# Kernel tuning notes

Measured on AMD Instinct MI355X. Metric: run time of the kernel, lower is better.

Reference implementation:

```python
import jax, jax.numpy as jnp
import numpy as np

NUM_CAPSULE = 10
DIM_CAPSULE = 16
NUM_ROUTING = 3
EPS = 1e-7  # tf.keras.backend.epsilon()


def squash(v, axis=-1):
    s2 = jnp.sum(jnp.square(v), axis=axis, keepdims=True)
    scale = s2 / (1.0 + s2) / jnp.sqrt(s2 + EPS)
    return scale * v


def setup_inputs() -> dict:
    key = jax.random.key(0)
    k1, k2 = jax.random.split(key)
    B, in_dim = 16384, 2048
    inputs = jax.random.normal(k1, (B, in_dim), dtype=jnp.float32)
    # glorot-uniform-ish scale for the kernel
    limit = np.sqrt(6.0 / (in_dim + NUM_CAPSULE * DIM_CAPSULE)).astype(np.float32)
    kernel = jax.random.uniform(k2, (in_dim, NUM_CAPSULE * DIM_CAPSULE),
                                dtype=jnp.float32, minval=-limit, maxval=limit)
    return {"inputs": inputs, "kernel": kernel}


def reference(inputs, kernel):
    B = inputs.shape[0]
    # [B, in_dim] @ [in_dim, nc*dc] -> [B, nc, dc]
    inputs_hat = (inputs @ kernel).reshape(B, NUM_CAPSULE, DIM_CAPSULE)
    b = jnp.zeros((B, NUM_CAPSULE, 1), dtype=inputs.dtype)
    outputs = None
    for _ in range(NUM_ROUTING):
        c = jax.nn.softmax(b, axis=1)                      # [B, nc, 1]
        s = jnp.sum(c * inputs_hat, axis=1, keepdims=True)  # [B, 1, dc]
        outputs = squash(s)                                 # [B, 1, dc]
        # matmul(inputs_hat, outputs, transpose_b=True) -> [B, nc, 1]
        b = b + jnp.einsum('bnd,bd->bn', inputs_hat, outputs[:, 0, :])[:, :, None]
    return outputs[:, 0, :]  # [B, dc]
```

## Files before the change

### kernel.cpp

```cpp
#include <hip/hip_runtime.h>
#include <hip/hip_bf16.h>

typedef unsigned int u32;
typedef unsigned short u16;
typedef __attribute__((ext_vector_type(8))) __bf16 bf16x8;
typedef __attribute__((ext_vector_type(4))) float f32x4;

#define N_CAP 10
#define D_CAP 16
#define NN 160
#define KK 2048
#define BM 64
#define BK 32
#define NSTEPS (KK / BK)
#define THREADS 640
#define LDST 40
#define AS_TILE (BM * LDST)
#define HAT_STRIDE 164
#define SMEM_BYTES (BM * HAT_STRIDE * 4)

__device__ __forceinline__ u32 pack_hi(float f0, float f1) {
  u32 u0 = __builtin_bit_cast(u32, f0), u1 = __builtin_bit_cast(u32, f1);
  return (u0 >> 16) | (u1 & 0xFFFF0000u);
}
__device__ __forceinline__ float hi_part(float f) {
  u32 u = __builtin_bit_cast(u32, f) & 0xFFFF0000u;
  return __builtin_bit_cast(float, u);
}
union U4B8 { uint4 u; bf16x8 b; };

__global__ __launch_bounds__(THREADS, 3) void capsule_fused(
    const float* __restrict__ X, const float* __restrict__ W, float* __restrict__ out) {
  __shared__ __align__(16) char smem[SMEM_BYTES];
  u16* As_hi = (u16*)smem;
  u16* As_lo = As_hi + AS_TILE;
  float* hat = (float*)smem;

  const int t = threadIdx.x;
  const int rbase = blockIdx.x * BM;
  const int lane = t & 63;
  const int w = t >> 6;
  const int wip = (w >= 5) ? 1 : 0;
  const int wjp = w - 5 * wip;
  const int l15 = lane & 15;
  const int q = lane >> 4;

  const int ar = t >> 2;
  const int ak = (t & 3) * 8;
  const float* gA = X + (size_t)(rbase + ar) * KK + ak;

  const float* gB = W + (q * 8) * NN + 32 * wjp + l15;

  f32x4 acc00 = {0.f,0.f,0.f,0.f}, acc01 = {0.f,0.f,0.f,0.f};
  f32x4 acc10 = {0.f,0.f,0.f,0.f}, acc11 = {0.f,0.f,0.f,0.f};

  float4 pa0A, pa1A, pa0B, pa1B;
  if (t < 256) {
    pa0A = *(const float4*)(gA);            pa1A = *(const float4*)(gA + 4);
    pa0B = *(const float4*)(gA + BK);       pa1B = *(const float4*)(gA + BK + 4);
  }
  float buA[16], buB[16];
#pragma unroll
  for (int j = 0; j < 8; ++j) { buA[j] = gB[j * NN]; buA[8 + j] = gB[16 + j * NN]; }

#define STEP(S, PA0, PA1, BU, BNXT)                                              \
  {                                                                              \
    __syncthreads();                            \
    if (t < 256) {                                                               \
      uint4 hi, lo;                                                              \
      hi.x = pack_hi(PA0.x, PA0.y); hi.y = pack_hi(PA0.z, PA0.w);                \
      hi.z = pack_hi(PA1.x, PA1.y); hi.w = pack_hi(PA1.z, PA1.w);                \
      float l0 = PA0.x - hi_part(PA0.x), l1 = PA0.y - hi_part(PA0.y);            \
      float l2 = PA0.z - hi_part(PA0.z), l3 = PA0.w - hi_part(PA0.w);            \
      float l4 = PA1.x - hi_part(PA1.x), l5 = PA1.y - hi_part(PA1.y);            \
      float l6 = PA1.z - hi_part(PA1.z), l7 = PA1.w - hi_part(PA1.w);            \
      lo.x = pack_hi(l0, l1); lo.y = pack_hi(l2, l3);                            \
      lo.z = pack_hi(l4, l5); lo.w = pack_hi(l6, l7);                            \
      *(uint4*)(As_hi + ar * LDST + ak) = hi;                                    \
      *(uint4*)(As_lo + ar * LDST + ak) = lo;                                    \
    }                                                                            \
    __syncthreads();                                             \
    if (t < 256 && (S) + 2 < NSTEPS) {                                           \
      PA0 = *(const float4*)(gA + ((S) + 2) * BK);                               \
      PA1 = *(const float4*)(gA + ((S) + 2) * BK + 4);                           \
    }                                                                            \
    if ((S) + 1 < NSTEPS) {                                                      \
      const float* b = gB + ((S) + 1) * (BK * NN);                               \
      _Pragma("unroll")                                                          \
      for (int j = 0; j < 8; ++j) { BNXT[j] = b[j * NN]; BNXT[8 + j] = b[16 + j * NN]; } \
    }                                                                            \
    U4B8 bh0, bl0, bh1, bl1;                                                     \
    bh0.u.x = pack_hi(BU[0], BU[1]);  bh0.u.y = pack_hi(BU[2], BU[3]);           \
    bh0.u.z = pack_hi(BU[4], BU[5]);  bh0.u.w = pack_hi(BU[6], BU[7]);           \
    bh1.u.x = pack_hi(BU[8], BU[9]);  bh1.u.y = pack_hi(BU[10], BU[11]);         \
    bh1.u.z = pack_hi(BU[12], BU[13]); bh1.u.w = pack_hi(BU[14], BU[15]);        \
    float lb[16];                                                                \
    _Pragma("unroll")                                                            \
    for (int j = 0; j < 16; ++j) lb[j] = BU[j] - hi_part(BU[j]);                 \
    bl0.u.x = pack_hi(lb[0], lb[1]);  bl0.u.y = pack_hi(lb[2], lb[3]);           \
    bl0.u.z = pack_hi(lb[4], lb[5]);  bl0.u.w = pack_hi(lb[6], lb[7]);           \
    bl1.u.x = pack_hi(lb[8], lb[9]);  bl1.u.y = pack_hi(lb[10], lb[11]);         \
    bl1.u.z = pack_hi(lb[12], lb[13]); bl1.u.w = pack_hi(lb[14], lb[15]);        \
    bf16x8 ah0 = *(const bf16x8*)(As_hi + (32 * wip + l15) * LDST + q * 8);      \
    bf16x8 ah1 = *(const bf16x8*)(As_hi + (32 * wip + 16 + l15) * LDST + q * 8); \
    bf16x8 al0 = *(const bf16x8*)(As_lo + (32 * wip + l15) * LDST + q * 8);      \
    bf16x8 al1 = *(const bf16x8*)(As_lo + (32 * wip + 16 + l15) * LDST + q * 8); \
    acc00 = __builtin_amdgcn_mfma_f32_16x16x32_bf16(ah0, bh0.b, acc00, 0, 0, 0); \
    acc00 = __builtin_amdgcn_mfma_f32_16x16x32_bf16(ah0, bl0.b, acc00, 0, 0, 0); \
    acc00 = __builtin_amdgcn_mfma_f32_16x16x32_bf16(al0, bh0.b, acc00, 0, 0, 0); \
    acc01 = __builtin_amdgcn_mfma_f32_16x16x32_bf16(ah0, bh1.b, acc01, 0, 0, 0); \
    acc01 = __builtin_amdgcn_mfma_f32_16x16x32_bf16(ah0, bl1.b, acc01, 0, 0, 0); \
    acc01 = __builtin_amdgcn_mfma_f32_16x16x32_bf16(al0, bh1.b, acc01, 0, 0, 0); \
    acc10 = __builtin_amdgcn_mfma_f32_16x16x32_bf16(ah1, bh0.b, acc10, 0, 0, 0); \
    acc10 = __builtin_amdgcn_mfma_f32_16x16x32_bf16(ah1, bl0.b, acc10, 0, 0, 0); \
    acc10 = __builtin_amdgcn_mfma_f32_16x16x32_bf16(al1, bh0.b, acc10, 0, 0, 0); \
    acc11 = __builtin_amdgcn_mfma_f32_16x16x32_bf16(ah1, bh1.b, acc11, 0, 0, 0); \
    acc11 = __builtin_amdgcn_mfma_f32_16x16x32_bf16(ah1, bl1.b, acc11, 0, 0, 0); \
    acc11 = __builtin_amdgcn_mfma_f32_16x16x32_bf16(al1, bh1.b, acc11, 0, 0, 0); \
  }

  for (int s = 0; s < NSTEPS; s += 2) {
    STEP(s,     pa0A, pa1A, buA, buB)
    STEP(s + 1, pa0B, pa1B, buB, buA)
  }
#undef STEP

  __syncthreads();
#pragma unroll
  for (int r = 0; r < 4; ++r) {
    const int rowb = 32 * wip + 4 * q + r;
    const int colb = 32 * wjp + l15;
    hat[rowb * HAT_STRIDE + colb]             = acc00[r];
    hat[rowb * HAT_STRIDE + colb + 16]        = acc01[r];
    hat[(rowb + 16) * HAT_STRIDE + colb]      = acc10[r];
    hat[(rowb + 16) * HAT_STRIDE + colb + 16] = acc11[r];
  }
  __syncthreads();

  if (t < BM) {
    const int r = t;
    float bb[N_CAP];
#pragma unroll
    for (int n = 0; n < N_CAP; ++n) bb[n] = 0.f;
    float v[D_CAP];
#pragma unroll
    for (int it = 0; it < 3; ++it) {
      float mx = bb[0];
#pragma unroll
      for (int n = 1; n < N_CAP; ++n) mx = fmaxf(mx, bb[n]);
      float c[N_CAP], se = 0.f;
#pragma unroll
      for (int n = 0; n < N_CAP; ++n) { c[n] = __expf(bb[n] - mx); se += c[n]; }
      const float inv = 1.f / se;
      float sd[D_CAP], s2 = 0.f;
#pragma unroll
      for (int d = 0; d < D_CAP; ++d) {
        float x = 0.f;
#pragma unroll
        for (int n = 0; n < N_CAP; ++n) x += c[n] * hat[r * HAT_STRIDE + n * D_CAP + d];
        x *= inv;
        sd[d] = x;
        s2 += x * x;
      }
      const float scale = s2 / ((1.f + s2) * sqrtf(s2 + 1e-7f));
#pragma unroll
      for (int d = 0; d < D_CAP; ++d) v[d] = scale * sd[d];
      if (it < 2) {
#pragma unroll
        for (int n = 0; n < N_CAP; ++n) {
          float dd = 0.f;
#pragma unroll
          for (int d = 0; d < D_CAP; ++d) dd += hat[r * HAT_STRIDE + n * D_CAP + d] * v[d];
          bb[n] += dd;
        }
      }
    }
#pragma unroll
    for (int d = 0; d < D_CAP; ++d)
      out[(size_t)(rbase + r) * D_CAP + d] = v[d];
  }
}

extern "C" void kernel_launch(void* const* d_in, const int* in_sizes, int n_in,
                              void* d_out, int out_size, void* d_ws, size_t ws_size,
                              hipStream_t stream) {
  const float* X = (const float*)d_in[0];
  const float* W = (const float*)d_in[1];
  if (n_in >= 2 && in_sizes[0] == KK * NN) {
    X = (const float*)d_in[1];
    W = (const float*)d_in[0];
  }
  capsule_fused<<<16384 / BM, THREADS, 0, stream>>>(X, W, (float*)d_out);
}
```

Baseline: 242.9 us.

## Prepack W into bf16 hi/lo fragments and load A directly without LDS

Adds a pre-kernel that splits W into bf16 hi/lo pairs laid out in MFMA fragment order in a global buffer, so the main kernel loads B fragments with vector loads instead of strided scalar loads and per-step packing. The A operand is now read per wave straight from global into registers, which removes the LDS staging and both barriers per k-step, at the cost of redundant A reads across the five column waves. The routing epilogue is spread over 8 threads per row using shuffle reductions, and occupancy hint drops to 2. The pack kernel runs on every call and adds a second launch.

```diff
diff --git a/kernel.cpp b/kernel.cpp
--- a/kernel.cpp
+++ b/kernel.cpp
@@ -1,5 +1,4 @@
 #include <hip/hip_runtime.h>
-#include <hip/hip_bf16.h>
 
 typedef unsigned int u32;
 typedef unsigned short u16;
@@ -11,13 +10,12 @@
 #define NN 160
 #define KK 2048
 #define BM 64
-#define BK 32
-#define NSTEPS (KK / BK)
+#define NSTEPS 64
 #define THREADS 640
-#define LDST 40
-#define AS_TILE (BM * LDST)
-#define HAT_STRIDE 164
-#define SMEM_BYTES (BM * HAT_STRIDE * 4)
+#define HAT_STRIDE 165
+#define BSTEP 20480
+
+__device__ __align__(16) unsigned char Wpack_g[NSTEPS * BSTEP];
 
 __device__ __forceinline__ u32 pack_hi(float f0, float f1) {
   u32 u0 = __builtin_bit_cast(u32, f0), u1 = __builtin_bit_cast(u32, f1);
@@ -29,12 +27,31 @@
 }
 union U4B8 { uint4 u; bf16x8 b; };
 
-__global__ __launch_bounds__(THREADS, 3) void capsule_fused(
-    const float* __restrict__ X, const float* __restrict__ W, float* __restrict__ out) {
-  __shared__ __align__(16) char smem[SMEM_BYTES];
-  u16* As_hi = (u16*)smem;
-  u16* As_lo = As_hi + AS_TILE;
-  float* hat = (float*)smem;
+__global__ void pack_w(const float* __restrict__ W) {
+  const int tid = blockIdx.x * 256 + threadIdx.x;
+  if (tid >= NSTEPS * 5 * 64 * 4) return;
+  const int v = tid & 3;
+  const int lane = (tid >> 2) & 63;
+  const int sw = tid >> 8;
+  const int wjp = sw % 5;
+  const int s = sw / 5;
+  const int col = 32 * wjp + 16 * (v & 1) + (lane & 15);
+  const int kb = 32 * s + 8 * (lane >> 4);
+  u32 r[4];
+#pragma unroll
+  for (int jj = 0; jj < 4; ++jj) {
+    float x0 = W[(size_t)(kb + 2 * jj) * NN + col];
+    float x1 = W[(size_t)(kb + 2 * jj + 1) * NN + col];
+    if (v >= 2) { x0 -= hi_part(x0); x1 -= hi_part(x1); }
+    r[jj] = pack_hi(x0, x1);
+  }
+  uint4 o; o.x = r[0]; o.y = r[1]; o.z = r[2]; o.w = r[3];
+  *(uint4*)(Wpack_g + (size_t)tid * 16) = o;
+}
+
+__global__ __launch_bounds__(THREADS, 2) void capsule_fused(
+    const float* __restrict__ X, float* __restrict__ out) {
+  __shared__ float hat[BM * HAT_STRIDE];
 
   const int t = threadIdx.x;
   const int rbase = blockIdx.x * BM;
@@ -45,87 +62,76 @@
   const int l15 = lane & 15;
   const int q = lane >> 4;
 
-  const int ar = t >> 2;
-  const int ak = (t & 3) * 8;
-  const float* gA = X + (size_t)(rbase + ar) * KK + ak;
-
-  const float* gB = W + (q * 8) * NN + 32 * wjp + l15;
+  const float* pA0 = X + (size_t)(rbase + 32 * wip + l15) * KK + 8 * q;
+  const float* pA1 = pA0 + 16 * KK;
+  const unsigned char* pB = Wpack_g + ((size_t)wjp * 64 + lane) * 64;
 
   f32x4 acc00 = {0.f,0.f,0.f,0.f}, acc01 = {0.f,0.f,0.f,0.f};
   f32x4 acc10 = {0.f,0.f,0.f,0.f}, acc11 = {0.f,0.f,0.f,0.f};
 
-  float4 pa0A, pa1A, pa0B, pa1B;
-  if (t < 256) {
-    pa0A = *(const float4*)(gA);            pa1A = *(const float4*)(gA + 4);
-    pa0B = *(const float4*)(gA + BK);       pa1B = *(const float4*)(gA + BK + 4);
-  }
-  float buA[16], buB[16];
-#pragma unroll
-  for (int j = 0; j < 8; ++j) { buA[j] = gB[j * NN]; buA[8 + j] = gB[16 + j * NN]; }
-
-#define STEP(S, PA0, PA1, BU, BNXT)                                              \
+  float4 aE0, aE1, aE2, aE3, aO0, aO1, aO2, aO3;
+  uint4 bE0, bE1, bE2, bE3, bO0, bO1, bO2, bO3;
+
+  aE0 = *(const float4*)(pA0);      aE1 = *(const float4*)(pA0 + 4);
+  aE2 = *(const float4*)(pA1);      aE3 = *(const float4*)(pA1 + 4);
+  aO0 = *(const float4*)(pA0 + 32); aO1 = *(const float4*)(pA0 + 36);
+  aO2 = *(const float4*)(pA1 + 32); aO3 = *(const float4*)(pA1 + 36);
+  bE0 = *(const uint4*)(pB);        bE1 = *(const uint4*)(pB + 16);
+  bE2 = *(const uint4*)(pB + 32);   bE3 = *(const uint4*)(pB + 48);
+
+#define STEP(S, A0, A1, A2, A3, BC0, BC1, BC2, BC3, BN0, BN1, BN2, BN3)          \
   {                                                                              \
-    __syncthreads();                            \
-    if (t < 256) {                                                               \
-      uint4 hi, lo;                                                              \
-      hi.x = pack_hi(PA0.x, PA0.y); hi.y = pack_hi(PA0.z, PA0.w);                \
-      hi.z = pack_hi(PA1.x, PA1.y); hi.w = pack_hi(PA1.z, PA1.w);                \
-      float l0 = PA0.x - hi_part(PA0.x), l1 = PA0.y - hi_part(PA0.y);            \
-      float l2 = PA0.z - hi_part(PA0.z), l3 = PA0.w - hi_part(PA0.w);            \
-      float l4 = PA1.x - hi_part(PA1.x), l5 = PA1.y - hi_part(PA1.y);            \
-      float l6 = PA1.z - hi_part(PA1.z), l7 = PA1.w - hi_part(PA1.w);            \
-      lo.x = pack_hi(l0, l1); lo.y = pack_hi(l2, l3);                            \
-      lo.z = pack_hi(l4, l5); lo.w = pack_hi(l6, l7);                            \
-      *(uint4*)(As_hi + ar * LDST + ak) = hi;                                    \
-      *(uint4*)(As_lo + ar * LDST + ak) = lo;                                    \
-    }                                                                            \
-    __syncthreads();                                             \
-    if (t < 256 && (S) + 2 < NSTEPS) {                                           \
-      PA0 = *(const float4*)(gA + ((S) + 2) * BK);                               \
-      PA1 = *(const float4*)(gA + ((S) + 2) * BK + 4);                           \
+    U4B8 ah0, al0, ah1, al1;                                                     \
+    ah0.u.x = pack_hi(A0.x, A0.y); ah0.u.y = pack_hi(A0.z, A0.w);                \
+    ah0.u.z = pack_hi(A1.x, A1.y); ah0.u.w = pack_hi(A1.z, A1.w);                \
+    { float l0 = A0.x - hi_part(A0.x), l1 = A0.y - hi_part(A0.y);                \
+      float l2 = A0.z - hi_part(A0.z), l3 = A0.w - hi_part(A0.w);                \
+      float l4 = A1.x - hi_part(A1.x), l5 = A1.y - hi_part(A1.y);                \
+      float l6 = A1.z - hi_part(A1.z), l7 = A1.w - hi_part(A1.w);                \
+      al0.u.x = pack_hi(l0, l1); al0.u.y = pack_hi(l2, l3);                      \
+      al0.u.z = pack_hi(l4, l5); al0.u.w = pack_hi(l6, l7); }                    \
+    ah1.u.x = pack_hi(A2.x, A2.y); ah1.u.y = pack_hi(A2.z, A2.w);                \
+    ah1.u.z = pack_hi(A3.x, A3.y); ah1.u.w = pack_hi(A3.z, A3.w);                \
+    { float l0 = A2.x - hi_part(A2.x), l1 = A2.y - hi_part(A2.y);                \
+      float l2 = A2.z - hi_part(A2.z), l3 = A2.w - hi_part(A2.w);                \
+      float l4 = A3.x - hi_part(A3.x), l5 = A3.y - hi_part(A3.y);                \
+      float l6 = A3.z - hi_part(A3.z), l7 = A3.w - hi_part(A3.w);                \
+      al1.u.x = pack_hi(l0, l1); al1.u.y = pack_hi(l2, l3);                      \
+      al1.u.z = pack_hi(l4, l5); al1.u.w = pack_hi(l6, l7); }                    \
+    if ((S) + 2 < NSTEPS) {                                                      \
+      A0 = *(const float4*)(pA0 + ((S) + 2) * 32);                               \
+      A1 = *(const float4*)(pA0 + ((S) + 2) * 32 + 4);                           \
+      A2 = *(const float4*)(pA1 + ((S) + 2) * 32);                               \
+      A3 = *(const float4*)(pA1 + ((S) + 2) * 32 + 4);                           \
     }                                                                            \
     if ((S) + 1 < NSTEPS) {                                                      \
-      const float* b = gB + ((S) + 1) * (BK * NN);                               \
-      _Pragma("unroll")                                                          \
-      for (int j = 0; j < 8; ++j) { BNXT[j] = b[j * NN]; BNXT[8 + j] = b[16 + j * NN]; } \
+      const unsigned char* bp = pB + ((size_t)((S) + 1)) * BSTEP;                \
+      BN0 = *(const uint4*)(bp);      BN1 = *(const uint4*)(bp + 16);            \
+      BN2 = *(const uint4*)(bp + 32); BN3 = *(const uint4*)(bp + 48);            \
     }                                                                            \
-    U4B8 bh0, bl0, bh1, bl1;                                                     \
-    bh0.u.x = pack_hi(BU[0], BU[1]);  bh0.u.y = pack_hi(BU[2], BU[3]);           \
-    bh0.u.z = pack_hi(BU[4], BU[5]);  bh0.u.w = pack_hi(BU[6], BU[7]);           \
-    bh1.u.x = pack_hi(BU[8], BU[9]);  bh1.u.y = pack_hi(BU[10], BU[11]);         \
-    bh1.u.z = pack_hi(BU[12], BU[13]); bh1.u.w = pack_hi(BU[14], BU[15]);        \
-    float lb[16];                                                                \
-    _Pragma("unroll")                                                            \
-    for (int j = 0; j < 16; ++j) lb[j] = BU[j] - hi_part(BU[j]);                 \
-    bl0.u.x = pack_hi(lb[0], lb[1]);  bl0.u.y = pack_hi(lb[2], lb[3]);           \
-    bl0.u.z = pack_hi(lb[4], lb[5]);  bl0.u.w = pack_hi(lb[6], lb[7]);           \
-    bl1.u.x = pack_hi(lb[8], lb[9]);  bl1.u.y = pack_hi(lb[10], lb[11]);         \
-    bl1.u.z = pack_hi(lb[12], lb[13]); bl1.u.w = pack_hi(lb[14], lb[15]);        \
-    bf16x8 ah0 = *(const bf16x8*)(As_hi + (32 * wip + l15) * LDST + q * 8);      \
-    bf16x8 ah1 = *(const bf16x8*)(As_hi + (32 * wip + 16 + l15) * LDST + q * 8); \
-    bf16x8 al0 = *(const bf16x8*)(As_lo + (32 * wip + l15) * LDST + q * 8);      \
-    bf16x8 al1 = *(const bf16x8*)(As_lo + (32 * wip + 16 + l15) * LDST + q * 8); \
-    acc00 = __builtin_amdgcn_mfma_f32_16x16x32_bf16(ah0, bh0.b, acc00, 0, 0, 0); \
-    acc00 = __builtin_amdgcn_mfma_f32_16x16x32_bf16(ah0, bl0.b, acc00, 0, 0, 0); \
-    acc00 = __builtin_amdgcn_mfma_f32_16x16x32_bf16(al0, bh0.b, acc00, 0, 0, 0); \
-    acc01 = __builtin_amdgcn_mfma_f32_16x16x32_bf16(ah0, bh1.b, acc01, 0, 0, 0); \
-    acc01 = __builtin_amdgcn_mfma_f32_16x16x32_bf16(ah0, bl1.b, acc01, 0, 0, 0); \
-    acc01 = __builtin_amdgcn_mfma_f32_16x16x32_bf16(al0, bh1.b, acc01, 0, 0, 0); \
-    acc10 = __builtin_amdgcn_mfma_f32_16x16x32_bf16(ah1, bh0.b, acc10, 0, 0, 0); \
-    acc10 = __builtin_amdgcn_mfma_f32_16x16x32_bf16(ah1, bl0.b, acc10, 0, 0, 0); \
-    acc10 = __builtin_amdgcn_mfma_f32_16x16x32_bf16(al1, bh0.b, acc10, 0, 0, 0); \
-    acc11 = __builtin_amdgcn_mfma_f32_16x16x32_bf16(ah1, bh1.b, acc11, 0, 0, 0); \
-    acc11 = __builtin_amdgcn_mfma_f32_16x16x32_bf16(ah1, bl1.b, acc11, 0, 0, 0); \
-    acc11 = __builtin_amdgcn_mfma_f32_16x16x32_bf16(al1, bh1.b, acc11, 0, 0, 0); \
-  }
-
+    U4B8 ub0, ub1, ub2, ub3;                                                     \
+    ub0.u = BC0; ub1.u = BC1; ub2.u = BC2; ub3.u = BC3;                          \
+    acc00 = __builtin_amdgcn_mfma_f32_16x16x32_bf16(ah0.b, ub0.b, acc00, 0,0,0); \
+    acc00 = __builtin_amdgcn_mfma_f32_16x16x32_bf16(ah0.b, ub2.b, acc00, 0,0,0); \
+    acc00 = __builtin_amdgcn_mfma_f32_16x16x32_bf16(al0.b, ub0.b, acc00, 0,0,0); \
+    acc01 = __builtin_amdgcn_mfma_f32_16x16x32_bf16(ah0.b, ub1.b, acc01, 0,0,0); \
+    acc01 = __builtin_amdgcn_mfma_f32_16x16x32_bf16(ah0.b, ub3.b, acc01, 0,0,0); \
+    acc01 = __builtin_amdgcn_mfma_f32_16x16x32_bf16(al0.b, ub1.b, acc01, 0,0,0); \
+    acc10 = __builtin_amdgcn_mfma_f32_16x16x32_bf16(ah1.b, ub0.b, acc10, 0,0,0); \
+    acc10 = __builtin_amdgcn_mfma_f32_16x16x32_bf16(ah1.b, ub2.b, acc10, 0,0,0); \
+    acc10 = __builtin_amdgcn_mfma_f32_16x16x32_bf16(al1.b, ub0.b, acc10, 0,0,0); \
+    acc11 = __builtin_amdgcn_mfma_f32_16x16x32_bf16(ah1.b, ub1.b, acc11, 0,0,0); \
+    acc11 = __builtin_amdgcn_mfma_f32_16x16x32_bf16(ah1.b, ub3.b, acc11, 0,0,0); \
+    acc11 = __builtin_amdgcn_mfma_f32_16x16x32_bf16(al1.b, ub1.b, acc11, 0,0,0); \
+  }
+
+#pragma unroll 1
   for (int s = 0; s < NSTEPS; s += 2) {
-    STEP(s,     pa0A, pa1A, buA, buB)
-    STEP(s + 1, pa0B, pa1B, buB, buA)
+    STEP(s,     aE0, aE1, aE2, aE3, bE0, bE1, bE2, bE3, bO0, bO1, bO2, bO3)
+    STEP(s + 1, aO0, aO1, aO2, aO3, bO0, bO1, bO2, bO3, bE0, bE1, bE2, bE3)
   }
 #undef STEP
 
-  __syncthreads();
 #pragma unroll
   for (int r = 0; r < 4; ++r) {
     const int rowb = 32 * wip + 4 * q + r;
@@ -137,12 +143,19 @@
   }
   __syncthreads();
 
-  if (t < BM) {
-    const int r = t;
+  if (t < BM * 8) {
+    const int r = t >> 3;
+    const int d0 = t & 7;
+    float h0[N_CAP], h1[N_CAP];
+#pragma unroll
+    for (int n = 0; n < N_CAP; ++n) {
+      h0[n] = hat[r * HAT_STRIDE + n * D_CAP + d0];
+      h1[n] = hat[r * HAT_STRIDE + n * D_CAP + d0 + 8];
+    }
     float bb[N_CAP];
 #pragma unroll
     for (int n = 0; n < N_CAP; ++n) bb[n] = 0.f;
-    float v[D_CAP];
+    float v0 = 0.f, v1 = 0.f;
 #pragma unroll
     for (int it = 0; it < 3; ++it) {
       float mx = bb[0];
@@ -152,32 +165,29 @@
 #pragma unroll
       for (int n = 0; n < N_CAP; ++n) { c[n] = __expf(bb[n] - mx); se += c[n]; }
       const float inv = 1.f / se;
-      float sd[D_CAP], s2 = 0.f;
-#pragma unroll
-      for (int d = 0; d < D_CAP; ++d) {
-        float x = 0.f;
-#pragma unroll
-        for (int n = 0; n < N_CAP; ++n) x += c[n] * hat[r * HAT_STRIDE + n * D_CAP + d];
-        x *= inv;
-        sd[d] = x;
-        s2 += x * x;
-      }
+      float s0 = 0.f, s1 = 0.f;
+#pragma unroll
+      for (int n = 0; n < N_CAP; ++n) { s0 += c[n] * h0[n]; s1 += c[n] * h1[n]; }
+      s0 *= inv; s1 *= inv;
+      float s2 = s0 * s0 + s1 * s1;
+      s2 += __shfl_xor(s2, 1);
+      s2 += __shfl_xor(s2, 2);
+      s2 += __shfl_xor(s2, 4);
       const float scale = s2 / ((1.f + s2) * sqrtf(s2 + 1e-7f));
-#pragma unroll
-      for (int d = 0; d < D_CAP; ++d) v[d] = scale * sd[d];
+      v0 = scale * s0; v1 = scale * s1;
       if (it < 2) {
 #pragma unroll
         for (int n = 0; n < N_CAP; ++n) {
-          float dd = 0.f;
-#pragma unroll
-          for (int d = 0; d < D_CAP; ++d) dd += hat[r * HAT_STRIDE + n * D_CAP + d] * v[d];
+          float dd = h0[n] * v0 + h1[n] * v1;
+          dd += __shfl_xor(dd, 1);
+          dd += __shfl_xor(dd, 2);
+          dd += __shfl_xor(dd, 4);
           bb[n] += dd;
         }
       }
     }
-#pragma unroll
-    for (int d = 0; d < D_CAP; ++d)
-      out[(size_t)(rbase + r) * D_CAP + d] = v[d];
+    out[(size_t)(rbase + r) * D_CAP + d0] = v0;
+    out[(size_t)(rbase + r) * D_CAP + d0 + 8] = v1;
   }
 }
 
@@ -190,5 +200,7 @@
     X = (const float*)d_in[1];
     W = (const float*)d_in[0];
   }
-  capsule_fused<<<16384 / BM, THREADS, 0, stream>>>(X, W, (float*)d_out);
-}
+  (void)d_ws; (void)ws_size; (void)out_size;
+  pack_w<<<(NSTEPS * 5 * 64 * 4 + 255) / 256, 256, 0, stream>>>(W);
+  capsule_fused<<<16384 / BM, THREADS, 0, stream>>>(X, (float*)d_out);
+}
```

New measurement: 282.1 us. +16.2%, slower.
